# Performance work log

Measured on AMD Instinct MI355X. Metric: run time of the kernel, lower is better.

Reference implementation:

```python
import jax, jax.numpy as jnp
import numpy as np
from jax import lax

EPS = 1e-5  # BatchNorm eps; eval-mode BN with running_mean=0, running_var=1


def _bn(v, g, b):
    return v * (g / jnp.sqrt(1.0 + EPS)) + b


def setup_inputs() -> dict:
    key = jax.random.key(0)
    ks = jax.random.split(key, 8)
    B, I, O, H, W, E, K, r = 16, 128, 128, 128, 128, 16, 3, 8
    Ir, Or = I // r, O // r
    f = jax.random.normal
    return {
        "x": f(ks[0], (B, I, H, W), jnp.float32),
        "experts": f(ks[1], (E, O, I, K, K), jnp.float32) * 0.05,
        "rw1": f(ks[2], (Ir, I), jnp.float32) * 0.05,
        "rbn1_g": jnp.ones((Ir,), jnp.float32),
        "rbn1_b": jnp.zeros((Ir,), jnp.float32),
        "rw2": f(ks[3], (I, Ir), jnp.float32) * 0.05,
        "rbn2_g": jnp.ones((I,), jnp.float32),
        "rbn2_b": jnp.zeros((I,), jnp.float32),
        "rw3": f(ks[4], (E, I), jnp.float32) * 0.05,
        "rb3": jnp.zeros((E,), jnp.float32),
        "ca_w1": f(ks[5], (Or, O), jnp.float32) * 0.05,
        "ca_bn1_g": jnp.ones((Or,), jnp.float32),
        "ca_bn1_b": jnp.zeros((Or,), jnp.float32),
        "ca_w2": f(ks[6], (O, Or), jnp.float32) * 0.05,
        "ca_bn2_g": jnp.ones((O,), jnp.float32),
        "ca_bn2_b": jnp.zeros((O,), jnp.float32),
        "sa_w": f(ks[7], (1, 2, 7, 7), jnp.float32) * 0.05,
        "sa_bn_g": jnp.ones((1,), jnp.float32),
        "sa_bn_b": jnp.zeros((1,), jnp.float32),
    }


def reference(x, experts, rw1, rbn1_g, rbn1_b, rw2, rbn2_g, rbn2_b, rw3, rb3,
              ca_w1, ca_bn1_g, ca_bn1_b, ca_w2, ca_bn2_g, ca_bn2_b,
              sa_w, sa_bn_g, sa_bn_b):
    B, I, H, W = x.shape
    E, O, _, K, _ = experts.shape
    # --- routing: avgpool -> 1x1 conv (matmul) -> BN -> ReLU -> 1x1 -> BN -> sigmoid -> 1x1 -> softmax
    p = jnp.mean(x, axis=(2, 3))                                  # [B, I]
    h = jax.nn.relu(_bn(p @ rw1.T, rbn1_g, rbn1_b))               # [B, I/r]
    g = jax.nn.sigmoid(_bn(h @ rw2.T, rbn2_g, rbn2_b))            # [B, I]
    rweights = jax.nn.softmax(g @ rw3.T + rb3, axis=1)            # [B, E]
    # --- expert-weighted kernel generation as a single GEMM
    w = jnp.einsum('be,eoihw->boihw', rweights, experts)          # [B, O, I, K, K]
    # --- per-sample conv via grouped conv (groups = B), stride=1, padding=1
    out = lax.conv_general_dilated(
        x.reshape(1, B * I, H, W),
        w.reshape(B * O, I, K, K),
        window_strides=(1, 1), padding=((1, 1), (1, 1)),
        dimension_numbers=('NCHW', 'OIHW', 'NCHW'),
        feature_group_count=B,
    ).reshape(B, O, H, W)
    # --- SE channel attention
    cp = jnp.mean(out, axis=(2, 3))                               # [B, O]
    ch = jax.nn.relu(_bn(cp @ ca_w1.T, ca_bn1_g, ca_bn1_b))
    cw = jax.nn.sigmoid(_bn(ch @ ca_w2.T, ca_bn2_g, ca_bn2_b))    # [B, O]
    out = out * cw[:, :, None, None]
    # --- CBAM spatial attention
    sp = jnp.concatenate([jnp.mean(out, axis=1, keepdims=True),
                          jnp.max(out, axis=1, keepdims=True)], axis=1)  # [B,2,H,W]
    sw = lax.conv_general_dilated(sp, sa_w, (1, 1), ((3, 3), (3, 3)),
                                  dimension_numbers=('NCHW', 'OIHW', 'NCHW'))
    sw = jax.nn.sigmoid(_bn(sw, sa_bn_g.reshape(1, 1, 1, 1), sa_bn_b.reshape(1, 1, 1, 1)))
    out = out * sw
    # --- residual (in_channels == out_channels -> Identity)
    return out + x
```

## Files before the change

kernel.cpp:

```cpp
#include <hip/hip_runtime.h>

typedef unsigned short ushort_t;
typedef __attribute__((ext_vector_type(4))) float float4_t;
typedef __attribute__((ext_vector_type(8))) short short8_t;
typedef __attribute__((ext_vector_type(8))) unsigned short ushort8_t;
typedef __attribute__((ext_vector_type(4))) unsigned short ushort4_t;

__device__ __forceinline__ ushort_t f2bf(float f) {
    unsigned u = __builtin_bit_cast(unsigned, f);
    u = (u + 0x7fffu + ((u >> 16) & 1u)) >> 16;
    return (ushort_t)u;
}
__device__ __forceinline__ ushort_t f2h(float f) {
    return __builtin_bit_cast(unsigned short, (_Float16)f);
}
__device__ __forceinline__ float h2f(ushort_t u) {
    return (float)__builtin_bit_cast(_Float16, u);
}

__device__ __forceinline__ void gld16(const void* g, void* l) {
    __builtin_amdgcn_global_load_lds(
        (const __attribute__((address_space(1))) unsigned int*)g,
        (__attribute__((address_space(3))) unsigned int*)l, 16, 0, 0);
}


__global__ __launch_bounds__(256) void init_kernel(float* __restrict__ p, float* __restrict__ cp,
                                                   float* __restrict__ sp, ushort_t* __restrict__ xn) {
    int t = blockIdx.x * 256 + threadIdx.x;
    if (t < 2048) { p[t] = 0.f; return; }
    if (t < 4096) { cp[t - 2048] = 0.f; return; }
    if (t < 4096 + 574592) { sp[t - 4096] = 0.f; return; }
    int e = t - (4096 + 574592);
    if (e < 1056768) {
        int b = e / 66048;
        int r = e % 66048;
        int pix = r >> 7, i = r & 127;
        int hp, wp;
        if (pix < 130)      { hp = 0;   wp = pix; }
        else if (pix < 260) { hp = 129; wp = pix - 130; }
        else { int q = pix - 260; hp = 1 + (q >> 1); wp = (q & 1) ? 129 : 0; }
        xn[((b * 130 + hp) * 130 + wp) * 128 + i] = 0;
    }
}

__global__ __launch_bounds__(256) void transpose_kernel(const float* __restrict__ x,
                                                        ushort_t* __restrict__ xn,
                                                        float* __restrict__ p) {
    __shared__ float tile[128][65];
    int blk = blockIdx.x;
    int wt = blk & 1, h = (blk >> 1) & 127, b = blk >> 8;
    int w0 = wt * 64;
    int tid = threadIdx.x;
    int wl = tid & 63, ig = tid >> 6;
    const float* src = x + ((long)(b * 128) * 128 + h) * 128 + w0 + wl;
    #pragma unroll
    for (int i = ig; i < 128; i += 4) tile[i][wl] = src[(long)i * 16384];
    __syncthreads();
    if (tid < 128) {
        float s = 0.f;
        #pragma unroll
        for (int w = 0; w < 64; ++w) s += tile[tid][w];
        atomicAdd(&p[b * 128 + tid], s * (1.0f / 16384.0f));
    }
    int l16 = tid & 15, wq = tid >> 4;
    #pragma unroll
    for (int pass = 0; pass < 4; ++pass) {
        int w = wq + pass * 16;
        ushort8_t v;
        #pragma unroll
        for (int j = 0; j < 8; ++j) v[j] = f2bf(tile[l16 * 8 + j][w]);
        *(ushort8_t*)&xn[((b * 130 + h + 1) * 130 + (w0 + w + 1)) * 128 + l16 * 8] = v;
    }
}

__global__ __launch_bounds__(256) void wgen_kernel(const float* __restrict__ experts,
        const float* __restrict__ p,
        const float* __restrict__ rw1, const float* __restrict__ g1, const float* __restrict__ b1,
        const float* __restrict__ rw2, const float* __restrict__ g2, const float* __restrict__ b2,
        const float* __restrict__ rw3, const float* __restrict__ rb3,
        ushort_t* __restrict__ w2) {
    int o = blockIdx.x;
    int tid = threadIdx.x;
    int lane = tid & 63, wave = tid >> 6;
    __shared__ __align__(16) float ex[16 * 1152];
    __shared__ float sg[16][128];
    __shared__ float sh[16][16];
    __shared__ float sl[16][16];
    __shared__ float rwl[16][16];

    const float* ebase = experts + (long)o * 1152;
    #pragma unroll
    for (int j = 0; j < 4; ++j) {
        int e = wave * 4 + j;
        const char* src = (const char*)(ebase + (long)e * 147456) + lane * 16;
        char* dst = (char*)&ex[e * 1152];
        #pragma unroll
        for (int k = 0; k < 5; ++k) {
            if (k < 4 || lane < 32)
                gld16(src + k * 1024, dst + k * 1024);
        }
    }

    const float bns = rsqrtf(1.0f + 1e-5f);
    {   int b = tid >> 4, j = tid & 15;
        float s = 0.f;
        for (int i = 0; i < 128; ++i) s += p[b * 128 + i] * rw1[j * 128 + i];
        s = s * (g1[j] * bns) + b1[j];
        sh[b][j] = fmaxf(s, 0.f); }
    __syncthreads();
    for (int c = 0; c < 8; ++c) {
        int idx = tid + c * 256;
        int b = idx >> 7, j = idx & 127;
        float s = 0.f;
        for (int k = 0; k < 16; ++k) s += sh[b][k] * rw2[j * 16 + k];
        s = s * (g2[j] * bns) + b2[j];
        sg[b][j] = 1.0f / (1.0f + expf(-s));
    }
    __syncthreads();
    {   int b = tid >> 4, e = tid & 15;
        float s = rb3[e];
        for (int j = 0; j < 128; ++j) s += sg[b][j] * rw3[e * 128 + j];
        sl[b][e] = s; }
    __syncthreads();
    {   int b = tid >> 4, e = tid & 15;
        float m = -1e30f;
        for (int k = 0; k < 16; ++k) m = fmaxf(m, sl[b][k]);
        float num = expf(sl[b][e] - m), den = 0.f;
        for (int k = 0; k < 16; ++k) den += expf(sl[b][k] - m);
        rwl[b][e] = num / den; }
    asm volatile("s_waitcnt vmcnt(0)" ::: "memory");
    __syncthreads();

    int i = tid & 127, half = tid >> 7;
    float acc[8][9];
    #pragma unroll
    for (int b = 0; b < 8; ++b)
        #pragma unroll
        for (int d = 0; d < 9; ++d) acc[b][d] = 0.f;
    for (int e = 0; e < 16; ++e) {
        float v[9];
        #pragma unroll
        for (int d = 0; d < 9; ++d) v[d] = ex[e * 1152 + i * 9 + d];
        #pragma unroll
        for (int b = 0; b < 8; ++b) {
            float r = rwl[half * 8 + b][e];
            #pragma unroll
            for (int d = 0; d < 9; ++d) acc[b][d] += v[d] * r;
        }
    }
    #pragma unroll
    for (int b = 0; b < 8; ++b)
        #pragma unroll
        for (int d = 0; d < 9; ++d)
            w2[(((half * 8 + b) * 9 + d) << 14) + (o << 7) + i] = f2bf(acc[b][d]);
}

struct __align__(16) ConvSmem {
    union {
        struct { ushort_t X[16640]; ushort_t A[4][4096]; } t;
        float c[4224];
    };
};

__global__ __launch_bounds__(256, 2) void conv_kernel(const ushort_t* __restrict__ xn,
                                                      const ushort_t* __restrict__ w2,
                                                      ushort_t* __restrict__ outi,
                                                      float* __restrict__ cp) {
    __shared__ ConvSmem sm;
    int bh = (blockIdx.x & 7) * 256 + (blockIdx.x >> 3);
    int b = bh >> 7, h = bh & 127;
    int tid = threadIdx.x;
    int lane = tid & 63, wave = tid >> 6;
    int wm = wave & 1, wn = wave >> 1;
    int q = lane >> 4, nl = lane & 15;

    float4_t acc[4][4];
    #pragma unroll
    for (int mi = 0; mi < 4; ++mi)
        #pragma unroll
        for (int ni = 0; ni < 4; ++ni) acc[mi][ni] = (float4_t){0.f, 0.f, 0.f, 0.f};

    const ushort_t* xbase = xn + (b * 130 + h) * 16640;
    const ushort_t* abase = w2 + (long)b * 147456;

    auto stageX = [&](int dy) {
        const ushort_t* xrow = xbase + dy * 16640;
        #pragma unroll
        for (int seg = wave; seg < 33; seg += 4) {
            if (seg < 32 || lane < 32) {
                int lofs = seg * 512 + lane * 8;
                int pp = lofs >> 7;
                int jb = (lofs & 127) >> 3;
                gld16(xrow + (pp << 7) + ((jb ^ (pp & 15)) << 3), &sm.t.X[seg * 512]);
            }
        }
    };
    auto stageA = [&](int c) {
        int dy = c / 12, rem = c % 12, dx = rem >> 2, ic = rem & 3;
        const ushort_t* ab = abase + (dy * 3 + dx) * 16384 + ic * 32;
        int buf = c & 3;
        int ol = lane >> 2;
        int jsrc = (lane & 3) ^ ((ol >> 1) & 3);
        #pragma unroll
        for (int inst = 0; inst < 2; ++inst) {
            int ob = wave * 32 + inst * 16;
            gld16(ab + (ob + ol) * 128 + (jsrc << 3), &sm.t.A[buf][ob * 32]);
        }
    };

    short8_t afr[2][4], bfr[2][4];
    auto readFrag = [&](int cc) {
        int pb = cc & 1;
        int dx = (cc % 12) >> 2, ic = cc & 3;
        const ushort_t* ap = &sm.t.A[cc & 3][0];
        #pragma unroll
        for (int mi = 0; mi < 4; ++mi) {
            int o = wm * 64 + mi * 16 + nl;
            afr[pb][mi] = *(const short8_t*)&ap[(o << 5) + ((q ^ ((o >> 1) & 3)) << 3)];
        }
        #pragma unroll
        for (int ni = 0; ni < 4; ++ni) {
            int pp = wn * 64 + ni * 16 + nl + dx;
            int J = ic * 4 + q;
            bfr[pb][ni] = *(const short8_t*)&sm.t.X[(pp << 7) + ((J ^ (pp & 15)) << 3)];
        }
    };
    auto domfma = [&](int pb) {
        __builtin_amdgcn_s_setprio(1);
        #pragma unroll
        for (int mi = 0; mi < 4; ++mi)
            #pragma unroll
            for (int ni = 0; ni < 4; ++ni)
                acc[mi][ni] = __builtin_amdgcn_mfma_f32_16x16x32_bf16(
                    afr[pb][mi], bfr[pb][ni], acc[mi][ni], 0, 0, 0);
        __builtin_amdgcn_s_setprio(0);
    };

    stageX(0);
    stageA(0); stageA(1); stageA(2);
    asm volatile("s_waitcnt vmcnt(0)" ::: "memory");
    __builtin_amdgcn_s_barrier();
    readFrag(0);

    #pragma unroll
    for (int c = 0; c < 36; ++c) {
        if (c + 3 < 36) stageA(c + 3);
        const bool bnd = (c == 11 || c == 23);
        if (!bnd && c + 1 < 36) readFrag(c + 1);
        domfma(c & 1);
        if (bnd) {
            __builtin_amdgcn_s_barrier();
            stageX(c == 11 ? 1 : 2);
            asm volatile("s_waitcnt vmcnt(0)" ::: "memory");
            __builtin_amdgcn_s_barrier();
            readFrag(c + 1);
        } else if (c < 35) {
            if (c == 33)
                asm volatile("s_waitcnt vmcnt(0)" ::: "memory");
            else if (!(c == 0 || c == 12 || c == 24 || c == 34))
                asm volatile("s_waitcnt vmcnt(2)" ::: "memory");
            __builtin_amdgcn_s_barrier();
        }
    }

    #pragma unroll
    for (int mi = 0; mi < 4; ++mi) {
        int o0 = wm * 64 + mi * 16 + q * 4;
        float rs[4] = {0.f, 0.f, 0.f, 0.f};
        #pragma unroll
        for (int ni = 0; ni < 4; ++ni) {
            float4_t v = acc[mi][ni];
            #pragma unroll
            for (int r = 0; r < 4; ++r) rs[r] += v[r];
        }
        #pragma unroll
        for (int r = 0; r < 4; ++r) {
            for (int msk = 1; msk < 16; msk <<= 1) rs[r] += __shfl_xor(rs[r], msk, 64);
            if (nl == 0) atomicAdd(&cp[(b << 7) + o0 + r], rs[r]);
        }
    }

    ushort_t* outb = outi + (((long)(b << 7)) << 14) + (h << 7);
    #pragma unroll
    for (int os = 0; os < 4; ++os) {
        __syncthreads();
        if (wm == (os >> 1)) {
            #pragma unroll
            for (int mi2 = 0; mi2 < 2; ++mi2) {
                int mi = (os & 1) * 2 + mi2;
                #pragma unroll
                for (int ni = 0; ni < 4; ++ni) {
                    float4_t v = acc[mi][ni];
                    int orow = mi2 * 16 + q * 4;
                    int w = wn * 64 + ni * 16 + nl;
                    #pragma unroll
                    for (int rr = 0; rr < 4; ++rr) sm.c[(orow + rr) * 132 + w] = v[rr];
                }
            }
        }
        __syncthreads();
        int row = tid >> 4, j = tid & 15;
        #pragma unroll
        for (int pass = 0; pass < 2; ++pass) {
            int r2 = pass * 16 + row;
            ushort8_t v;
            #pragma unroll
            for (int k = 0; k < 8; ++k) v[k] = f2h(sm.c[r2 * 132 + j * 8 + k]);
            *(ushort8_t*)&outb[((long)(os * 32 + r2) << 14) + j * 8] = v;
        }
    }
}

__global__ __launch_bounds__(256) void stat_kernel(const ushort_t* __restrict__ outi,
        const float* __restrict__ cp,
        const float* __restrict__ w1, const float* __restrict__ g1, const float* __restrict__ b1,
        const float* __restrict__ w2, const float* __restrict__ g2, const float* __restrict__ b2,
        float* __restrict__ cw, float* __restrict__ sp) {
    int b = blockIdx.x >> 7, h = blockIdx.x & 127;
    int tid = threadIdx.x;
    __shared__ float scp[128], sch[16], scw[128];
    __shared__ float ssum[4][128], smax[4][128];
    const float bns = rsqrtf(1.0f + 1e-5f);
    if (tid < 128) scp[tid] = cp[(b << 7) + tid] * (1.0f / 16384.0f);
    __syncthreads();
    if (tid < 16) {
        float s = 0.f;
        for (int o = 0; o < 128; ++o) s += scp[o] * w1[tid * 128 + o];
        s = s * (g1[tid] * bns) + b1[tid];
        sch[tid] = fmaxf(s, 0.f);
    }
    __syncthreads();
    if (tid < 128) {
        float s = 0.f;
        #pragma unroll
        for (int k = 0; k < 16; ++k) s += sch[k] * w2[tid * 16 + k];
        s = s * (g2[tid] * bns) + b2[tid];
        scw[tid] = 1.0f / (1.0f + expf(-s));
        if (h == 0) cw[(b << 7) + tid] = scw[tid];
    }
    __syncthreads();
    int wp = (tid & 63) << 1, og = tid >> 6;
    const ushort_t* src = outi + ((long)b << 21) + ((long)(og << 5) << 14) + (h << 7) + wp;
    float s0 = 0.f, s1 = 0.f, m0 = -1e30f, m1 = -1e30f;
    #pragma unroll 8
    for (int o = 0; o < 32; ++o) {
        unsigned u = *(const unsigned*)&src[(long)o << 14];
        float c = scw[(og << 5) + o];
        float v0 = h2f((ushort_t)(u & 0xffffu)) * c;
        float v1 = h2f((ushort_t)(u >> 16)) * c;
        s0 += v0; s1 += v1;
        m0 = fmaxf(m0, v0); m1 = fmaxf(m1, v1);
    }
    ssum[og][wp] = s0; ssum[og][wp + 1] = s1;
    smax[og][wp] = m0; smax[og][wp + 1] = m1;
    __syncthreads();
    if (tid < 128) {
        float s = ssum[0][tid] + ssum[1][tid] + ssum[2][tid] + ssum[3][tid];
        float m = fmaxf(fmaxf(smax[0][tid], smax[1][tid]),
                        fmaxf(smax[2][tid], smax[3][tid]));
        float* d = sp + b * 2 * 17956;
        d[(h + 3) * 134 + (tid + 3)] = s * (1.0f / 128.0f);
        d[17956 + (h + 3) * 134 + (tid + 3)] = m;
    }
}

__global__ __launch_bounds__(256) void sattn_kernel(const float* __restrict__ sp,
        const float* __restrict__ k98, const float* __restrict__ g, const float* __restrict__ bb,
        const float* __restrict__ cw, const float* __restrict__ x,
        const ushort_t* __restrict__ outi, float* __restrict__ out) {
    int b = blockIdx.x >> 7, h = blockIdx.x & 127;
    int tid = threadIdx.x;
    __shared__ float ls[2][7][134];
    __shared__ float lk[98];
    __shared__ float sws[128];
    __shared__ float scw[128];
    const float* sb = sp + b * 2 * 17956;
    for (int idx = tid; idx < 2 * 7 * 134; idx += 256) {
        int c = idx / 938, rr = idx % 938;
        int ky = rr / 134, wp = rr % 134;
        ls[c][ky][wp] = sb[c * 17956 + (h + ky) * 134 + wp];
    }
    if (tid < 98) lk[tid] = k98[tid];
    if (tid >= 128) scw[tid - 128] = cw[(b << 7) + (tid - 128)];
    __syncthreads();
    if (tid < 128) {
        float s = 0.f;
        #pragma unroll
        for (int c = 0; c < 2; ++c)
            #pragma unroll
            for (int ky = 0; ky < 7; ++ky)
                #pragma unroll
                for (int kx = 0; kx < 7; ++kx)
                    s += ls[c][ky][tid + kx] * lk[c * 49 + ky * 7 + kx];
        s = s * (g[0] * rsqrtf(1.0f + 1e-5f)) + bb[0];
        sws[tid] = 1.0f / (1.0f + expf(-s));
    }
    __syncthreads();
    int w4 = tid & 31, og = tid >> 5;
    long base = (((long)b << 21) + (h << 7)) + (w4 << 2);
    float4_t sv = *(const float4_t*)&sws[w4 << 2];
    #pragma unroll
    for (int o = og; o < 128; o += 8) {
        long idx = base + ((long)o << 14);
        ushort4_t hv = *(const ushort4_t*)&outi[idx];
        float4_t ov = (float4_t){h2f(hv[0]), h2f(hv[1]), h2f(hv[2]), h2f(hv[3])};
        float4_t xv = *(const float4_t*)&x[idx];
        float4_t r = ov * scw[o] * sv + xv;
        *(float4_t*)&out[idx] = r;
    }
}

extern "C" void kernel_launch(void* const* d_in, const int* in_sizes, int n_in,
                              void* d_out, int out_size, void* d_ws, size_t ws_size,
                              hipStream_t stream) {
    const float* x       = (const float*)d_in[0];
    const float* experts = (const float*)d_in[1];
    const float* rw1     = (const float*)d_in[2];
    const float* rbn1_g  = (const float*)d_in[3];
    const float* rbn1_b  = (const float*)d_in[4];
    const float* rw2     = (const float*)d_in[5];
    const float* rbn2_g  = (const float*)d_in[6];
    const float* rbn2_b  = (const float*)d_in[7];
    const float* rw3     = (const float*)d_in[8];
    const float* rb3     = (const float*)d_in[9];
    const float* ca_w1   = (const float*)d_in[10];
    const float* ca_bn1g = (const float*)d_in[11];
    const float* ca_bn1b = (const float*)d_in[12];
    const float* ca_w2   = (const float*)d_in[13];
    const float* ca_bn2g = (const float*)d_in[14];
    const float* ca_bn2b = (const float*)d_in[15];
    const float* sa_w    = (const float*)d_in[16];
    const float* sa_g    = (const float*)d_in[17];
    const float* sa_b    = (const float*)d_in[18];
    float* out = (float*)d_out;
    char* ws = (char*)d_ws;

    ushort_t* xn   = (ushort_t*)(ws);
    ushort_t* w2   = (ushort_t*)(ws + 69222400);
    float*    p    = (float*)(ws + 73940992);
    float*    cp   = (float*)(ws + 73949184);
    float*    cw   = (float*)(ws + 73958400);
    float*    sp   = (float*)(ws + 73966592);
    ushort_t* outi = (ushort_t*)(ws + 76264960);

    hipLaunchKernelGGL(init_kernel, dim3(6389), dim3(256), 0, stream, p, cp, sp, xn);
    hipLaunchKernelGGL(transpose_kernel, dim3(4096), dim3(256), 0, stream, x, xn, p);
    hipLaunchKernelGGL(wgen_kernel, dim3(128), dim3(256), 0, stream,
                       experts, p, rw1, rbn1_g, rbn1_b, rw2, rbn2_g, rbn2_b, rw3, rb3, w2);
    hipLaunchKernelGGL(conv_kernel, dim3(2048), dim3(256), 0, stream, xn, w2, outi, cp);
    hipLaunchKernelGGL(stat_kernel, dim3(2048), dim3(256), 0, stream,
                       outi, cp, ca_w1, ca_bn1g, ca_bn1b, ca_w2, ca_bn2g, ca_bn2b, cw, sp);
    hipLaunchKernelGGL(sattn_kernel, dim3(2048), dim3(256), 0, stream,
                       sp, sa_w, sa_g, sa_b, cw, x, outi, out);
}
```

Before: 465.1 us.

## Compute SE channel means analytically from input border sums, fuse spatial stats into conv

The per-channel mean of the conv output is computed algebraically from the generated weights and from per-channel input totals, row, column and corner border sums gathered in the transpose kernel, instead of being reduced from conv accumulators. This lets the SE attention weights be computed in a tiny kernel before the conv, so the conv epilogue can apply them and produce the spatial mean/max maps directly. The separate stat kernel that re-read the whole fp16 conv output is removed. The cost is extra atomics in the transpose kernel, a single-block SE kernel on the critical path, and channel means taken from fp32 weights rather than from the bf16 conv result.

```diff
diff --git a/kernel.cpp b/kernel.cpp
--- a/kernel.cpp
+++ b/kernel.cpp
@@ -25,13 +25,13 @@
 }
 
 
-__global__ __launch_bounds__(256) void init_kernel(float* __restrict__ p, float* __restrict__ cp,
+__global__ __launch_bounds__(256) void init_kernel(float* __restrict__ p, float* __restrict__ st,
                                                    float* __restrict__ sp, ushort_t* __restrict__ xn) {
     int t = blockIdx.x * 256 + threadIdx.x;
     if (t < 2048) { p[t] = 0.f; return; }
-    if (t < 4096) { cp[t - 2048] = 0.f; return; }
-    if (t < 4096 + 574592) { sp[t - 4096] = 0.f; return; }
-    int e = t - (4096 + 574592);
+    if (t < 18432) { st[t - 2048] = 0.f; return; }
+    if (t < 18432 + 574592) { sp[t - 18432] = 0.f; return; }
+    int e = t - (18432 + 574592);
     if (e < 1056768) {
         int b = e / 66048;
         int r = e % 66048;
@@ -46,7 +46,8 @@
 
 __global__ __launch_bounds__(256) void transpose_kernel(const float* __restrict__ x,
                                                         ushort_t* __restrict__ xn,
-                                                        float* __restrict__ p) {
+                                                        float* __restrict__ p,
+                                                        float* __restrict__ st) {
     __shared__ float tile[128][65];
     int blk = blockIdx.x;
     int wt = blk & 1, h = (blk >> 1) & 127, b = blk >> 8;
@@ -62,6 +63,13 @@
         #pragma unroll
         for (int w = 0; w < 64; ++w) s += tile[tid][w];
         atomicAdd(&p[b * 128 + tid], s * (1.0f / 16384.0f));
+        float* sb = st + ((b << 7) + tid) * 8;
+        if (h == 0)   atomicAdd(&sb[0], s);
+        if (h == 127) atomicAdd(&sb[1], s);
+        float edge = tile[tid][wt ? 63 : 0];
+        atomicAdd(&sb[wt ? 3 : 2], edge);
+        if (h == 0)   sb[wt ? 5 : 4] = edge;
+        if (h == 127) sb[wt ? 7 : 6] = edge;
     }
     int l16 = tid & 15, wq = tid >> 4;
     #pragma unroll
@@ -75,11 +83,11 @@
 }
 
 __global__ __launch_bounds__(256) void wgen_kernel(const float* __restrict__ experts,
-        const float* __restrict__ p,
+        const float* __restrict__ p, const float* __restrict__ st,
         const float* __restrict__ rw1, const float* __restrict__ g1, const float* __restrict__ b1,
         const float* __restrict__ rw2, const float* __restrict__ g2, const float* __restrict__ b2,
         const float* __restrict__ rw3, const float* __restrict__ rb3,
-        ushort_t* __restrict__ w2) {
+        ushort_t* __restrict__ w2, float* __restrict__ cp) {
     int o = blockIdx.x;
     int tid = threadIdx.x;
     int lane = tid & 63, wave = tid >> 6;
@@ -88,6 +96,7 @@
     __shared__ float sh[16][16];
     __shared__ float sl[16][16];
     __shared__ float rwl[16][16];
+    __shared__ float cpw[4][8];
 
     const float* ebase = experts + (long)o * 1152;
     #pragma unroll
@@ -149,11 +158,73 @@
             for (int d = 0; d < 9; ++d) acc[b][d] += v[d] * r;
         }
     }
+    float cps[8];
+    #pragma unroll
+    for (int bb2 = 0; bb2 < 8; ++bb2) {
+        int b = half * 8 + bb2;
+        const float* sb = st + ((b << 7) + i) * 8;
+        float T = p[(b << 7) + i] * 16384.f;
+        float r0 = sb[0], r127 = sb[1], c0 = sb[2], c127 = sb[3];
+        float x00 = sb[4], x0127 = sb[5], x1270 = sb[6], x127127 = sb[7];
+        float S0 = T - r127 - c127 + x127127;
+        float S1 = T - r127;
+        float S2 = T - r127 - c0 + x1270;
+        float S3 = T - c127;
+        float S4 = T;
+        float S5 = T - c0;
+        float S6 = T - r0 - c127 + x0127;
+        float S7 = T - r0;
+        float S8 = T - r0 - c0 + x00;
+        cps[bb2] = acc[bb2][0] * S0 + acc[bb2][1] * S1 + acc[bb2][2] * S2 +
+                   acc[bb2][3] * S3 + acc[bb2][4] * S4 + acc[bb2][5] * S5 +
+                   acc[bb2][6] * S6 + acc[bb2][7] * S7 + acc[bb2][8] * S8;
+    }
+    #pragma unroll
+    for (int bb2 = 0; bb2 < 8; ++bb2)
+        for (int msk = 1; msk < 64; msk <<= 1) cps[bb2] += __shfl_xor(cps[bb2], msk, 64);
+    if (lane == 0) {
+        #pragma unroll
+        for (int bb2 = 0; bb2 < 8; ++bb2) cpw[wave][bb2] = cps[bb2];
+    }
     #pragma unroll
     for (int b = 0; b < 8; ++b)
         #pragma unroll
         for (int d = 0; d < 9; ++d)
             w2[(((half * 8 + b) * 9 + d) << 14) + (o << 7) + i] = f2bf(acc[b][d]);
+    __syncthreads();
+    if (tid < 16) {
+        int hf = tid >> 3, idx = tid & 7;
+        cp[(tid << 7) + o] = cpw[hf * 2][idx] + cpw[hf * 2 + 1][idx];
+    }
+}
+
+__global__ __launch_bounds__(256) void se_kernel(const float* __restrict__ cp,
+        const float* __restrict__ w1, const float* __restrict__ g1, const float* __restrict__ b1,
+        const float* __restrict__ w2, const float* __restrict__ g2, const float* __restrict__ b2,
+        float* __restrict__ cw) {
+    __shared__ float sc[16][128];
+    __shared__ float sh[16][16];
+    int tid = threadIdx.x;
+    const float bns = rsqrtf(1.0f + 1e-5f);
+    for (int c = 0; c < 8; ++c) {
+        int idx = tid + c * 256;
+        sc[idx >> 7][idx & 127] = cp[idx] * (1.0f / 16384.0f);
+    }
+    __syncthreads();
+    {   int b = tid >> 4, j = tid & 15;
+        float s = 0.f;
+        for (int o = 0; o < 128; ++o) s += sc[b][o] * w1[j * 128 + o];
+        s = s * (g1[j] * bns) + b1[j];
+        sh[b][j] = fmaxf(s, 0.f); }
+    __syncthreads();
+    for (int c = 0; c < 8; ++c) {
+        int idx = tid + c * 256;
+        int b = idx >> 7, o = idx & 127;
+        float s = 0.f;
+        for (int k = 0; k < 16; ++k) s += sh[b][k] * w2[o * 16 + k];
+        s = s * (g2[o] * bns) + b2[o];
+        cw[idx] = 1.0f / (1.0f + expf(-s));
+    }
 }
 
 struct __align__(16) ConvSmem {
@@ -165,9 +236,12 @@
 
 __global__ __launch_bounds__(256, 2) void conv_kernel(const ushort_t* __restrict__ xn,
                                                       const ushort_t* __restrict__ w2,
+                                                      const float* __restrict__ cw,
                                                       ushort_t* __restrict__ outi,
-                                                      float* __restrict__ cp) {
+                                                      float* __restrict__ sp) {
     __shared__ ConvSmem sm;
+    __shared__ float scw[128];
+    __shared__ float cmb[2][128];
     int bh = (blockIdx.x & 7) * 256 + (blockIdx.x >> 3);
     int b = bh >> 7, h = bh & 127;
     int tid = threadIdx.x;
@@ -183,6 +257,9 @@
 
     const ushort_t* xbase = xn + (b * 130 + h) * 16640;
     const ushort_t* abase = w2 + (long)b * 147456;
+
+    float cwv = 0.f;
+    if (tid < 128) cwv = cw[(b << 7) + tid];
 
     auto stageX = [&](int dy) {
         const ushort_t* xrow = xbase + dy * 16640;
@@ -239,6 +316,7 @@
 
     stageX(0);
     stageA(0); stageA(1); stageA(2);
+    if (tid < 128) scw[tid] = cwv;
     asm volatile("s_waitcnt vmcnt(0)" ::: "memory");
     __builtin_amdgcn_s_barrier();
     readFrag(0);
@@ -264,24 +342,9 @@
         }
     }
 
-    #pragma unroll
-    for (int mi = 0; mi < 4; ++mi) {
-        int o0 = wm * 64 + mi * 16 + q * 4;
-        float rs[4] = {0.f, 0.f, 0.f, 0.f};
-        #pragma unroll
-        for (int ni = 0; ni < 4; ++ni) {
-            float4_t v = acc[mi][ni];
-            #pragma unroll
-            for (int r = 0; r < 4; ++r) rs[r] += v[r];
-        }
-        #pragma unroll
-        for (int r = 0; r < 4; ++r) {
-            for (int msk = 1; msk < 16; msk <<= 1) rs[r] += __shfl_xor(rs[r], msk, 64);
-            if (nl == 0) atomicAdd(&cp[(b << 7) + o0 + r], rs[r]);
-        }
-    }
-
     ushort_t* outb = outi + (((long)(b << 7)) << 14) + (h << 7);
+    int wpx = tid & 127, g = tid >> 7;
+    float wsum = 0.f, wmax = -1e30f;
     #pragma unroll
     for (int os = 0; os < 4; ++os) {
         __syncthreads();
@@ -309,59 +372,22 @@
             for (int k = 0; k < 8; ++k) v[k] = f2h(sm.c[r2 * 132 + j * 8 + k]);
             *(ushort8_t*)&outb[((long)(os * 32 + r2) << 14) + j * 8] = v;
         }
-    }
-}
-
-__global__ __launch_bounds__(256) void stat_kernel(const ushort_t* __restrict__ outi,
-        const float* __restrict__ cp,
-        const float* __restrict__ w1, const float* __restrict__ g1, const float* __restrict__ b1,
-        const float* __restrict__ w2, const float* __restrict__ g2, const float* __restrict__ b2,
-        float* __restrict__ cw, float* __restrict__ sp) {
-    int b = blockIdx.x >> 7, h = blockIdx.x & 127;
-    int tid = threadIdx.x;
-    __shared__ float scp[128], sch[16], scw[128];
-    __shared__ float ssum[4][128], smax[4][128];
-    const float bns = rsqrtf(1.0f + 1e-5f);
-    if (tid < 128) scp[tid] = cp[(b << 7) + tid] * (1.0f / 16384.0f);
-    __syncthreads();
-    if (tid < 16) {
-        float s = 0.f;
-        for (int o = 0; o < 128; ++o) s += scp[o] * w1[tid * 128 + o];
-        s = s * (g1[tid] * bns) + b1[tid];
-        sch[tid] = fmaxf(s, 0.f);
-    }
-    __syncthreads();
-    if (tid < 128) {
-        float s = 0.f;
-        #pragma unroll
-        for (int k = 0; k < 16; ++k) s += sch[k] * w2[tid * 16 + k];
-        s = s * (g2[tid] * bns) + b2[tid];
-        scw[tid] = 1.0f / (1.0f + expf(-s));
-        if (h == 0) cw[(b << 7) + tid] = scw[tid];
-    }
-    __syncthreads();
-    int wp = (tid & 63) << 1, og = tid >> 6;
-    const ushort_t* src = outi + ((long)b << 21) + ((long)(og << 5) << 14) + (h << 7) + wp;
-    float s0 = 0.f, s1 = 0.f, m0 = -1e30f, m1 = -1e30f;
-    #pragma unroll 8
-    for (int o = 0; o < 32; ++o) {
-        unsigned u = *(const unsigned*)&src[(long)o << 14];
-        float c = scw[(og << 5) + o];
-        float v0 = h2f((ushort_t)(u & 0xffffu)) * c;
-        float v1 = h2f((ushort_t)(u >> 16)) * c;
-        s0 += v0; s1 += v1;
-        m0 = fmaxf(m0, v0); m1 = fmaxf(m1, v1);
-    }
-    ssum[og][wp] = s0; ssum[og][wp + 1] = s1;
-    smax[og][wp] = m0; smax[og][wp + 1] = m1;
-    __syncthreads();
-    if (tid < 128) {
-        float s = ssum[0][tid] + ssum[1][tid] + ssum[2][tid] + ssum[3][tid];
-        float m = fmaxf(fmaxf(smax[0][tid], smax[1][tid]),
-                        fmaxf(smax[2][tid], smax[3][tid]));
+        #pragma unroll
+        for (int r = 0; r < 16; ++r) {
+            int orow = g * 16 + r;
+            float v = sm.c[orow * 132 + wpx] * scw[os * 32 + orow];
+            wsum += v;
+            wmax = fmaxf(wmax, v);
+        }
+    }
+    if (g == 1) { cmb[0][wpx] = wsum; cmb[1][wpx] = wmax; }
+    __syncthreads();
+    if (g == 0) {
+        wsum += cmb[0][wpx];
+        wmax = fmaxf(wmax, cmb[1][wpx]);
         float* d = sp + b * 2 * 17956;
-        d[(h + 3) * 134 + (tid + 3)] = s * (1.0f / 128.0f);
-        d[17956 + (h + 3) * 134 + (tid + 3)] = m;
+        d[(h + 3) * 134 + (wpx + 3)] = wsum * (1.0f / 128.0f);
+        d[17956 + (h + 3) * 134 + (wpx + 3)] = wmax;
     }
 }
 
@@ -443,14 +469,16 @@
     float*    cw   = (float*)(ws + 73958400);
     float*    sp   = (float*)(ws + 73966592);
     ushort_t* outi = (ushort_t*)(ws + 76264960);
-
-    hipLaunchKernelGGL(init_kernel, dim3(6389), dim3(256), 0, stream, p, cp, sp, xn);
-    hipLaunchKernelGGL(transpose_kernel, dim3(4096), dim3(256), 0, stream, x, xn, p);
+    float*    st   = (float*)(ws + 143373824);
+
+    hipLaunchKernelGGL(init_kernel, dim3(6445), dim3(256), 0, stream, p, st, sp, xn);
+    hipLaunchKernelGGL(transpose_kernel, dim3(4096), dim3(256), 0, stream, x, xn, p, st);
     hipLaunchKernelGGL(wgen_kernel, dim3(128), dim3(256), 0, stream,
-                       experts, p, rw1, rbn1_g, rbn1_b, rw2, rbn2_g, rbn2_b, rw3, rb3, w2);
-    hipLaunchKernelGGL(conv_kernel, dim3(2048), dim3(256), 0, stream, xn, w2, outi, cp);
-    hipLaunchKernelGGL(stat_kernel, dim3(2048), dim3(256), 0, stream,
-                       outi, cp, ca_w1, ca_bn1g, ca_bn1b, ca_w2, ca_bn2g, ca_bn2b, cw, sp);
+                       experts, p, st, rw1, rbn1_g, rbn1_b, rw2, rbn2_g, rbn2_b, rw3, rb3,
+                       w2, cp);
+    hipLaunchKernelGGL(se_kernel, dim3(1), dim3(256), 0, stream,
+                       cp, ca_w1, ca_bn1g, ca_bn1b, ca_w2, ca_bn2g, ca_bn2b, cw);
+    hipLaunchKernelGGL(conv_kernel, dim3(2048), dim3(256), 0, stream, xn, w2, cw, outi, sp);
     hipLaunchKernelGGL(sattn_kernel, dim3(2048), dim3(256), 0, stream,
                        sp, sa_w, sa_g, sa_b, cw, x, outi, out);
 }
```

Result: no change. 469.0 us (+0.8%).
